# Kernel tuning notes

Hardware: AMD Instinct MI355X
Metric: run time of the kernel (lower is better)

Reference implementation:

```python
import jax, jax.numpy as jnp
import numpy as np

B, T, D_MODEL, N_HEAD = 2, 2048, 1024, 16
HEAD_DIM = D_MODEL // N_HEAD


def setup_inputs() -> dict:
    key = jax.random.key(0)
    ks = jax.random.split(key, 4)
    s = 0.02
    return {
        "x": jax.random.normal(ks[0], (B, T, D_MODEL), dtype=jnp.float32),
        "freqs_cis": jnp.zeros((T, HEAD_DIM // 2), dtype=jnp.float32),  # unused under ALiBi
        "Wq": jax.random.normal(ks[1], (D_MODEL, D_MODEL), dtype=jnp.float32) * s,
        "bq": jnp.zeros((D_MODEL,), dtype=jnp.float32),
        "Wkv": jax.random.normal(ks[2], (2 * D_MODEL, D_MODEL), dtype=jnp.float32) * s,
        "bkv": jnp.zeros((2 * D_MODEL,), dtype=jnp.float32),
        "Wo": jax.random.normal(ks[3], (D_MODEL, D_MODEL), dtype=jnp.float32) * s,
        "bo": jnp.zeros((D_MODEL,), dtype=jnp.float32),
    }


def reference(x, freqs_cis, Wq, bq, Wkv, bkv, Wo, bo):
    Bb, Tt, C = x.shape
    H, Dh = N_HEAD, HEAD_DIM
    # projections (torch Linear: x @ W^T + b)
    q = (x @ Wq.T + bq).reshape(Bb, Tt, H, Dh).transpose(0, 2, 1, 3)      # [B,H,T,Dh]
    kv = (x @ Wkv.T + bkv).reshape(Bb, Tt, 2, H, Dh).transpose(2, 0, 3, 1, 4)
    k, v = kv[0], kv[1]                                                    # [B,H,T,Dh]
    scores = jnp.einsum('bhqd,bhkd->bhqk', q, k) * (1.0 / np.sqrt(Dh))
    # ALiBi: linear slopes (1/H ... 1.0), bias = slope * (j - i)
    slopes = jnp.arange(1, H + 1, dtype=jnp.float32) / H                   # [H]
    pos = jnp.arange(Tt, dtype=jnp.float32)
    dist = pos[None, :] - pos[:, None]                                     # [T,T], j - i
    scores = scores + slopes[:, None, None] * dist[None]                   # broadcast over B
    # causal mask (upper triangle -> -inf)
    causal = pos[:, None] >= pos[None, :]                                  # [T,T] keep-mask
    scores = jnp.where(causal[None, None], scores, -jnp.inf)
    attn = jax.nn.softmax(scores, axis=-1)
    y = jnp.einsum('bhqk,bhkd->bhqd', attn, v)                             # [B,H,T,Dh]
    y = y.transpose(0, 2, 1, 3).reshape(Bb, Tt, C)
    return y @ Wo.T + bo
```

## Files before the change

kernel.cpp:

```cpp
#include <hip/hip_runtime.h>

typedef unsigned short u16;
typedef __bf16 bf16x8 __attribute__((ext_vector_type(8)));
typedef unsigned short u16x8 __attribute__((ext_vector_type(8)));
typedef float f32x4 __attribute__((ext_vector_type(4)));

#define KEY(r) ((((r) ^ ((r) >> 3)) & 7) << 3)
#define GP 72
#define VKEY(d) ((((d) >> 3) & 7) << 3)

static __device__ __forceinline__ u16 f2b(float f) {
  union { float f; unsigned u; } x; x.f = f;
  unsigned r = x.u + 0x7FFFu + ((x.u >> 16) & 1u);
  return (u16)(r >> 16);
}

static __device__ __forceinline__ float b2f(u16 s) {
  union { unsigned u; float f; } z; z.u = (unsigned)s << 16; return z.f;
}

static __device__ __forceinline__ bf16x8 ld_frag(const u16* p) {
  union { u16x8 s; bf16x8 b; } u;
  u.s = *reinterpret_cast<const u16x8*>(p);
  return u.b;
}

__global__ __launch_bounds__(256) void cvt_f32_bf16(const float* __restrict__ in,
                                                    u16* __restrict__ out, int n4) {
  int i = blockIdx.x * 256 + threadIdx.x;
  if (i >= n4) return;
  float4 v = reinterpret_cast<const float4*>(in)[i];
  ushort4 o;
  o.x = f2b(v.x); o.y = f2b(v.y); o.z = f2b(v.z); o.w = f2b(v.w);
  reinterpret_cast<ushort4*>(out)[i] = o;
}

template <bool OUT_BF16, int BN>
static __device__ __forceinline__ void gemm_body(
    const u16* __restrict__ A, const u16* __restrict__ Bt,
    const float* __restrict__ bias, void* __restrict__ outp,
    int N, int K, int row0, int col0, float scale) {
  constexpr int NF = BN / 32;
  __shared__ alignas(16) u16 As[128 * 64];
  __shared__ alignas(16) u16 Bs[BN * 64];
  const int tid = threadIdx.x, wid = tid >> 6, lane = tid & 63;
  const int wr = wid >> 1, wc = wid & 1;
  const int lr = lane >> 3;
  const int lc = (lane & 7) * 8;
  const int frow = lane & 15, fk = (lane >> 4) * 8;
  f32x4 acc[4][NF] = {};

  for (int k0 = 0; k0 < K; k0 += 64) {
    __syncthreads();
#pragma unroll
    for (int t = 0; t < 4; ++t) {
      const int r = wid * 32 + t * 8 + lr;
      __builtin_amdgcn_global_load_lds(
          (const __attribute__((address_space(1))) unsigned int*)(
              A + (size_t)(row0 + r) * K + k0 + (lc ^ KEY(r))),
          (__attribute__((address_space(3))) unsigned int*)(As + (wid * 32 + t * 8) * 64),
          16, 0, 0);
    }
#pragma unroll
    for (int t = 0; t < NF; ++t) {
      const int r = wid * (BN / 4) + t * 8 + lr;
      __builtin_amdgcn_global_load_lds(
          (const __attribute__((address_space(1))) unsigned int*)(
              Bt + (size_t)(col0 + r) * K + k0 + (lc ^ KEY(r))),
          (__attribute__((address_space(3))) unsigned int*)(Bs + (wid * (BN / 4) + t * 8) * 64),
          16, 0, 0);
    }
    __syncthreads();
#pragma unroll
    for (int ks = 0; ks < 2; ++ks) {
      bf16x8 a[4], b[NF];
#pragma unroll
      for (int m = 0; m < 4; ++m) {
        const int r = wr * 64 + m * 16 + frow;
        a[m] = ld_frag(&As[r * 64 + ((ks * 32 + fk) ^ KEY(r))]);
      }
#pragma unroll
      for (int n = 0; n < NF; ++n) {
        const int r = wc * (BN / 2) + n * 16 + frow;
        b[n] = ld_frag(&Bs[r * 64 + ((ks * 32 + fk) ^ KEY(r))]);
      }
#pragma unroll
      for (int m = 0; m < 4; ++m)
#pragma unroll
        for (int n = 0; n < NF; ++n)
          acc[m][n] = __builtin_amdgcn_mfma_f32_16x16x32_bf16(a[m], b[n], acc[m][n], 0, 0, 0);
    }
  }
  const int colL = lane & 15, rb = (lane >> 4) * 4;
#pragma unroll
  for (int n = 0; n < NF; ++n) {
    const int gc = col0 + wc * (BN / 2) + n * 16 + colL;
    const float bv = bias[gc];
#pragma unroll
    for (int m = 0; m < 4; ++m)
#pragma unroll
      for (int r = 0; r < 4; ++r) {
        const int gr = row0 + wr * 64 + m * 16 + rb + r;
        const float v = (acc[m][n][r] + bv) * scale;
        if constexpr (OUT_BF16)
          reinterpret_cast<u16*>(outp)[(size_t)gr * N + gc] = f2b(v);
        else
          reinterpret_cast<float*>(outp)[(size_t)gr * N + gc] = v;
      }
  }
}

__global__ __launch_bounds__(256) void gemm_qkv(
    const u16* __restrict__ xb, const u16* __restrict__ wqb,
    const u16* __restrict__ wkvb, const float* __restrict__ bq,
    const float* __restrict__ bkv, u16* __restrict__ qb, u16* __restrict__ kvb) {
  const int row0 = blockIdx.x * 128;
  const int by = blockIdx.y;
  const u16* Bt; const float* bias; u16* out; int N, col0; float scale;
  if (by < 8) { Bt = wqb;  bias = bq;  out = qb;  N = 1024; col0 = by * 128;      scale = 0.125f; }
  else        { Bt = wkvb; bias = bkv; out = kvb; N = 2048; col0 = (by - 8) * 128; scale = 1.0f; }
  gemm_body<true, 128>(xb, Bt, bias, out, N, 1024, row0, col0, scale);
}

__global__ __launch_bounds__(256) void gemm_o(
    const u16* __restrict__ yb, const u16* __restrict__ wob,
    const float* __restrict__ bo, float* __restrict__ out) {
  gemm_body<false, 64>(yb, wob, bo, out, 1024, 1024, blockIdx.x * 128, blockIdx.y * 64, 1.0f);
}

__global__ __launch_bounds__(256) void attn_split(
    const u16* __restrict__ qb,
    const u16* __restrict__ kvb,
    u16* __restrict__ yb,
    char* __restrict__ part,
    int T) {
  const int C = 1024;
  const int bh = blockIdx.x;
  const int b = bh >> 4, h = bh & 15;
  const float slope = (float)(h + 1) * 0.0625f;
  const int tid = threadIdx.x, wid = tid >> 6, lane = tid & 63;

  const int y = blockIdx.y;
  int qt, t0, t1, pidx; bool direct;
  if (y < 32) {
    qt = 31 - (y >> 1);
    const int c = y & 1, nt = qt + 1, half = (nt + 1) >> 1;
    t0 = c ? half : 0; t1 = c ? nt : half;
    direct = false;
    pidx = ((bh << 4) + (qt - 16)) * 2 + c;
  } else {
    qt = 47 - y; t0 = 0; t1 = qt + 1; direct = true; pidx = 0;
  }
  const int qBase = qt * 64;

  __shared__ alignas(16) u16 Ks[64 * GP];
  __shared__ alignas(16) u16 Vt[64 * GP];
  __shared__ alignas(16) u16 Ps[4][16 * GP];

  const int frow = lane & 15, fk = (lane >> 4) * 8;
  const int col = lane & 15, rb = (lane >> 4) * 4;

  const int q_row = qBase + wid * 16 + frow;
  const u16* qp = qb + (size_t)(b * T + q_row) * C + h * 64;
  const bf16x8 aq0 = ld_frag(qp + fk);
  const bf16x8 aq1 = ld_frag(qp + 32 + fk);

  float mrow[4] = {-1e30f, -1e30f, -1e30f, -1e30f};
  float lrow[4] = {0.f, 0.f, 0.f, 0.f};
  f32x4 accO[4] = {};

  const int sr = tid >> 3;
  const int sc = (tid & 7) * 8;

  for (int kt = t0; kt < t1; ++kt) {
    const int kBase = kt * 64;
    __syncthreads();
    {
      const size_t g0 = (size_t)(b * T + kBase + sr) * 2048 + h * 64 + sc;
      const size_t g1 = (size_t)(b * T + kBase + sr + 32) * 2048 + h * 64 + sc;
      *reinterpret_cast<int4*>(&Ks[sr * GP + sc]) = *reinterpret_cast<const int4*>(&kvb[g0]);
      *reinterpret_cast<int4*>(&Ks[(sr + 32) * GP + sc]) = *reinterpret_cast<const int4*>(&kvb[g1]);
      int4 v0 = *reinterpret_cast<const int4*>(&kvb[g0 + 1024]);
      int4 v1 = *reinterpret_cast<const int4*>(&kvb[g1 + 1024]);
      const u16* p0 = reinterpret_cast<const u16*>(&v0);
      const u16* p1 = reinterpret_cast<const u16*>(&v1);
      const int kx = VKEY(sc);
#pragma unroll
      for (int j = 0; j < 8; ++j) {
        const int d = sc + j;
        Vt[d * GP + (sr ^ kx)] = p0[j];
        Vt[d * GP + ((sr + 32) ^ kx)] = p1[j];
      }
    }
    __syncthreads();

    f32x4 accS[4] = {};
#pragma unroll
    for (int n = 0; n < 4; ++n) {
      bf16x8 bk0 = ld_frag(&Ks[(n * 16 + frow) * GP + fk]);
      accS[n] = __builtin_amdgcn_mfma_f32_16x16x32_bf16(aq0, bk0, accS[n], 0, 0, 0);
      bf16x8 bk1 = ld_frag(&Ks[(n * 16 + frow) * GP + 32 + fk]);
      accS[n] = __builtin_amdgcn_mfma_f32_16x16x32_bf16(aq1, bk1, accS[n], 0, 0, 0);
    }

#pragma unroll
    for (int r = 0; r < 4; ++r) {
      const int qg = qBase + wid * 16 + rb + r;
      float s[4];
      float tmax = -1e30f;
#pragma unroll
      for (int n = 0; n < 4; ++n) {
        const int kg = kBase + n * 16 + col;
        float v = accS[n][r] + slope * (float)(kg - qg);
        if (kg > qg) v = -1e30f;
        s[n] = v;
        tmax = fmaxf(tmax, v);
      }
      tmax = fmaxf(tmax, __shfl_xor(tmax, 1));
      tmax = fmaxf(tmax, __shfl_xor(tmax, 2));
      tmax = fmaxf(tmax, __shfl_xor(tmax, 4));
      tmax = fmaxf(tmax, __shfl_xor(tmax, 8));
      const float newm = fmaxf(mrow[r], tmax);
      const float corr = __expf(mrow[r] - newm);
      mrow[r] = newm;
      float psum = 0.f;
#pragma unroll
      for (int n = 0; n < 4; ++n) {
        const float p = __expf(s[n] - newm);
        psum += p;
        Ps[wid][(rb + r) * GP + n * 16 + col] = f2b(p);
      }
      psum += __shfl_xor(psum, 1);
      psum += __shfl_xor(psum, 2);
      psum += __shfl_xor(psum, 4);
      psum += __shfl_xor(psum, 8);
      lrow[r] = lrow[r] * corr + psum;
#pragma unroll
      for (int n = 0; n < 4; ++n) accO[n][r] *= corr;
    }

#pragma unroll
    for (int ks = 0; ks < 2; ++ks) {
      bf16x8 ap = ld_frag(&Ps[wid][frow * GP + ks * 32 + fk]);
#pragma unroll
      for (int n = 0; n < 4; ++n) {
        const int d = n * 16 + frow;
        bf16x8 bv = ld_frag(&Vt[d * GP + ((ks * 32 + fk) ^ VKEY(d))]);
        accO[n] = __builtin_amdgcn_mfma_f32_16x16x32_bf16(ap, bv, accO[n], 0, 0, 0);
      }
    }
  }

  if (direct) {
#pragma unroll
    for (int r = 0; r < 4; ++r) {
      const float inv = 1.0f / lrow[r];
      const int qg = qBase + wid * 16 + rb + r;
      u16* yrow = yb + (size_t)(b * T + qg) * C + h * 64;
#pragma unroll
      for (int n = 0; n < 4; ++n) yrow[n * 16 + col] = f2b(accO[n][r] * inv);
    }
  } else {
    u16* Orec = (u16*)(part + (size_t)pidx * 8704);
    float* mrec = (float*)(part + (size_t)pidx * 8704 + 8192);
#pragma unroll
    for (int r = 0; r < 4; ++r) {
      const int row = wid * 16 + rb + r;
#pragma unroll
      for (int n = 0; n < 4; ++n)
        Orec[row * 64 + n * 16 + col] = f2b(accO[n][r]);
      if (col == 0) { mrec[row] = mrow[r]; mrec[64 + row] = lrow[r]; }
    }
  }
}

__global__ __launch_bounds__(256) void attn_combine(
    const char* __restrict__ part, u16* __restrict__ yb, int T) {
  const int C = 1024;
  const int bh = blockIdx.x, b = bh >> 4, h = bh & 15;
  const int qt = 16 + blockIdx.y;
  const int tid = threadIdx.x;
  const int row = tid >> 2;
  const int d0 = (tid & 3) * 16;
  const size_t base = (size_t)(((bh << 4) + (qt - 16)) * 2) * 8704;
  const char* r0 = part + base;
  const char* r1 = part + base + 8704;
  const float m0 = ((const float*)(r0 + 8192))[row];
  const float l0 = ((const float*)(r0 + 8192))[64 + row];
  const float m1 = ((const float*)(r1 + 8192))[row];
  const float l1 = ((const float*)(r1 + 8192))[64 + row];
  const float M = fmaxf(m0, m1);
  const float w0 = __expf(m0 - M), w1 = __expf(m1 - M);
  const float inv = 1.0f / (l0 * w0 + l1 * w1);
  const u16* o0 = (const u16*)r0 + row * 64 + d0;
  const u16* o1 = (const u16*)r1 + row * 64 + d0;
  alignas(16) u16 outv[16];
#pragma unroll
  for (int j = 0; j < 16; ++j)
    outv[j] = f2b((b2f(o0[j]) * w0 + b2f(o1[j]) * w1) * inv);
  u16* yrow = yb + (size_t)(b * T + qt * 64 + row) * C + h * 64 + d0;
  *reinterpret_cast<int4*>(yrow) = *reinterpret_cast<const int4*>(outv);
  *reinterpret_cast<int4*>(yrow + 8) = *reinterpret_cast<const int4*>(outv + 8);
}

extern "C" void kernel_launch(void* const* d_in, const int* in_sizes, int n_in,
                              void* d_out, int out_size, void* d_ws, size_t ws_size,
                              hipStream_t stream) {
  const float* x   = (const float*)d_in[0];
  const float* Wq  = (const float*)d_in[2];
  const float* bq  = (const float*)d_in[3];
  const float* Wkv = (const float*)d_in[4];
  const float* bkv = (const float*)d_in[5];
  const float* Wo  = (const float*)d_in[6];
  const float* bo  = (const float*)d_in[7];
  float* out = (float*)d_out;

  const int B = 2, T = 2048, C = 1024;
  const int M = B * T;

  char* ws = (char*)d_ws;
  u16* xb   = (u16*)(ws + 0);
  u16* wqb  = (u16*)(ws + 8388608);
  u16* wkvb = (u16*)(ws + 10485760);
  u16* wob  = (u16*)(ws + 14680064);
  u16* qb   = (u16*)(ws + 16777216);
  u16* kvb  = (u16*)(ws + 25165824);
  u16* yb   = (u16*)(ws + 41943040);
  char* part = ws;

  cvt_f32_bf16<<<(M * C / 4 + 255) / 256, 256, 0, stream>>>(x, xb, M * C / 4);
  cvt_f32_bf16<<<(C * C / 4 + 255) / 256, 256, 0, stream>>>(Wq, wqb, C * C / 4);
  cvt_f32_bf16<<<(2 * C * C / 4 + 255) / 256, 256, 0, stream>>>(Wkv, wkvb, 2 * C * C / 4);
  cvt_f32_bf16<<<(C * C / 4 + 255) / 256, 256, 0, stream>>>(Wo, wob, C * C / 4);

  gemm_qkv<<<dim3(M / 128, 8 + 16), 256, 0, stream>>>(xb, wqb, wkvb, bq, bkv, qb, kvb);
  attn_split<<<dim3(B * 16, 48), 256, 0, stream>>>(qb, kvb, yb, part, T);
  attn_combine<<<dim3(B * 16, 16), 256, 0, stream>>>(part, yb, T);
  gemm_o<<<dim3(M / 128, C / 64), 256, 0, stream>>>(yb, wob, bo, out);
}
```

Measured before the change: 243.2 us.

## Transpose score MFMA to per-lane query rows and drop split-K combine

The score MFMA now takes swapped operands so each lane owns a single query row. Row max and sum then need only two cross-lane shuffles, and the bf16 P tile is packed into 32-bit shared-memory words instead of being stored one element at a time. The ALiBi term drops the -slope*q part, which is constant per row and cancels in softmax. The split-KV path plus its separate combine kernel are removed and replaced by one block per query tile, which brings back load imbalance on the long causal tiles in exchange for dropping the partial writes and an extra launch.

New measurement: 213.8 us. -12.1%, faster.

```diff
diff --git a/kernel.cpp b/kernel.cpp
--- a/kernel.cpp
+++ b/kernel.cpp
@@ -1,6 +1,7 @@
 #include <hip/hip_runtime.h>
 
 typedef unsigned short u16;
+typedef unsigned int u32;
 typedef __bf16 bf16x8 __attribute__((ext_vector_type(8)));
 typedef unsigned short u16x8 __attribute__((ext_vector_type(8)));
 typedef float f32x4 __attribute__((ext_vector_type(4)));
@@ -13,10 +14,6 @@
   union { float f; unsigned u; } x; x.f = f;
   unsigned r = x.u + 0x7FFFu + ((x.u >> 16) & 1u);
   return (u16)(r >> 16);
-}
-
-static __device__ __forceinline__ float b2f(u16 s) {
-  union { unsigned u; float f; } z; z.u = (unsigned)s << 16; return z.f;
 }
 
 static __device__ __forceinline__ bf16x8 ld_frag(const u16* p) {
@@ -128,51 +125,41 @@
   gemm_body<false, 64>(yb, wob, bo, out, 1024, 1024, blockIdx.x * 128, blockIdx.y * 64, 1.0f);
 }
 
-__global__ __launch_bounds__(256) void attn_split(
+__global__ __launch_bounds__(256) void attn_kernel(
     const u16* __restrict__ qb,
     const u16* __restrict__ kvb,
     u16* __restrict__ yb,
-    char* __restrict__ part,
     int T) {
   const int C = 1024;
   const int bh = blockIdx.x;
+  const int qt = (int)gridDim.y - 1 - (int)blockIdx.y;
   const int b = bh >> 4, h = bh & 15;
   const float slope = (float)(h + 1) * 0.0625f;
   const int tid = threadIdx.x, wid = tid >> 6, lane = tid & 63;
-
-  const int y = blockIdx.y;
-  int qt, t0, t1, pidx; bool direct;
-  if (y < 32) {
-    qt = 31 - (y >> 1);
-    const int c = y & 1, nt = qt + 1, half = (nt + 1) >> 1;
-    t0 = c ? half : 0; t1 = c ? nt : half;
-    direct = false;
-    pidx = ((bh << 4) + (qt - 16)) * 2 + c;
-  } else {
-    qt = 47 - y; t0 = 0; t1 = qt + 1; direct = true; pidx = 0;
-  }
   const int qBase = qt * 64;
 
   __shared__ alignas(16) u16 Ks[64 * GP];
   __shared__ alignas(16) u16 Vt[64 * GP];
-  __shared__ alignas(16) u16 Ps[4][16 * GP];
-
-  const int frow = lane & 15, fk = (lane >> 4) * 8;
-  const int col = lane & 15, rb = (lane >> 4) * 4;
-
-  const int q_row = qBase + wid * 16 + frow;
+  __shared__ alignas(16) u32 Pl[4][16 * 40];
+
+  const int qc = lane & 15;
+  const int g  = lane >> 4;
+  const int g4 = g * 4;
+  const int fk = g * 8;
+
+  const int q_row = qBase + wid * 16 + qc;
   const u16* qp = qb + (size_t)(b * T + q_row) * C + h * 64;
   const bf16x8 aq0 = ld_frag(qp + fk);
   const bf16x8 aq1 = ld_frag(qp + 32 + fk);
-
-  float mrow[4] = {-1e30f, -1e30f, -1e30f, -1e30f};
-  float lrow[4] = {0.f, 0.f, 0.f, 0.f};
+  const int qg = q_row;
+
+  float m_q = -1e30f, l_q = 0.f;
   f32x4 accO[4] = {};
 
   const int sr = tid >> 3;
   const int sc = (tid & 7) * 8;
 
-  for (int kt = t0; kt < t1; ++kt) {
+  for (int kt = 0; kt <= qt; ++kt) {
     const int kBase = kt * 64;
     __syncthreads();
     {
@@ -197,110 +184,84 @@
     f32x4 accS[4] = {};
 #pragma unroll
     for (int n = 0; n < 4; ++n) {
-      bf16x8 bk0 = ld_frag(&Ks[(n * 16 + frow) * GP + fk]);
-      accS[n] = __builtin_amdgcn_mfma_f32_16x16x32_bf16(aq0, bk0, accS[n], 0, 0, 0);
-      bf16x8 bk1 = ld_frag(&Ks[(n * 16 + frow) * GP + 32 + fk]);
-      accS[n] = __builtin_amdgcn_mfma_f32_16x16x32_bf16(aq1, bk1, accS[n], 0, 0, 0);
-    }
-
-#pragma unroll
-    for (int r = 0; r < 4; ++r) {
-      const int qg = qBase + wid * 16 + rb + r;
-      float s[4];
-      float tmax = -1e30f;
+      bf16x8 bk0 = ld_frag(&Ks[(n * 16 + qc) * GP + fk]);
+      accS[n] = __builtin_amdgcn_mfma_f32_16x16x32_bf16(bk0, aq0, accS[n], 0, 0, 0);
+      bf16x8 bk1 = ld_frag(&Ks[(n * 16 + qc) * GP + 32 + fk]);
+      accS[n] = __builtin_amdgcn_mfma_f32_16x16x32_bf16(bk1, aq1, accS[n], 0, 0, 0);
+    }
+
+    float tmax = -1e30f;
+#pragma unroll
+    for (int n = 0; n < 4; ++n) {
+      const int kgn = kBase + n * 16 + g4;
+#pragma unroll
+      for (int r = 0; r < 4; ++r) {
+        const int kg = kgn + r;
+        float v = fmaf(slope, (float)kg, accS[n][r]);
+        v = (kg > qg) ? -1e30f : v;
+        accS[n][r] = v;
+        tmax = fmaxf(tmax, v);
+      }
+    }
+    tmax = fmaxf(tmax, __shfl_xor(tmax, 16));
+    tmax = fmaxf(tmax, __shfl_xor(tmax, 32));
+    const float newm = fmaxf(m_q, tmax);
+    const float corr = __expf(m_q - newm);
+    m_q = newm;
+    float psum = 0.f;
+#pragma unroll
+    for (int n = 0; n < 4; ++n)
+#pragma unroll
+      for (int r = 0; r < 4; ++r) {
+        const float p = __expf(accS[n][r] - newm);
+        accS[n][r] = p;
+        psum += p;
+      }
+    psum += __shfl_xor(psum, 16);
+    psum += __shfl_xor(psum, 32);
+    l_q = l_q * corr + psum;
+
+    u32* Pw = &Pl[wid][qc * 40];
+#pragma unroll
+    for (int n = 0; n < 4; ++n) {
+      union { float f; u32 u; } a0, a1, a2, a3;
+      a0.f = accS[n][0]; a1.f = accS[n][1]; a2.f = accS[n][2]; a3.f = accS[n][3];
+      u32 w0 = (a0.u >> 16) | (a1.u & 0xFFFF0000u);
+      u32 w1 = (a2.u >> 16) | (a3.u & 0xFFFF0000u);
+      *reinterpret_cast<uint2*>(&Pw[8 * n + 2 * g]) = uint2{w0, w1};
+    }
+
+    float corr4[4];
+#pragma unroll
+    for (int r = 0; r < 4; ++r) corr4[r] = __shfl(corr, g4 + r);
+#pragma unroll
+    for (int n = 0; n < 4; ++n)
+#pragma unroll
+      for (int r = 0; r < 4; ++r) accO[n][r] *= corr4[r];
+
+#pragma unroll
+    for (int ks = 0; ks < 2; ++ks) {
+      uint4 pv4 = *reinterpret_cast<const uint4*>(&Pl[wid][qc * 40 + 16 * ks + g4]);
+      union { uint4 q; u16x8 s; bf16x8 bv; } ap; ap.q = pv4;
 #pragma unroll
       for (int n = 0; n < 4; ++n) {
-        const int kg = kBase + n * 16 + col;
-        float v = accS[n][r] + slope * (float)(kg - qg);
-        if (kg > qg) v = -1e30f;
-        s[n] = v;
-        tmax = fmaxf(tmax, v);
-      }
-      tmax = fmaxf(tmax, __shfl_xor(tmax, 1));
-      tmax = fmaxf(tmax, __shfl_xor(tmax, 2));
-      tmax = fmaxf(tmax, __shfl_xor(tmax, 4));
-      tmax = fmaxf(tmax, __shfl_xor(tmax, 8));
-      const float newm = fmaxf(mrow[r], tmax);
-      const float corr = __expf(mrow[r] - newm);
-      mrow[r] = newm;
-      float psum = 0.f;
-#pragma unroll
-      for (int n = 0; n < 4; ++n) {
-        const float p = __expf(s[n] - newm);
-        psum += p;
-        Ps[wid][(rb + r) * GP + n * 16 + col] = f2b(p);
-      }
-      psum += __shfl_xor(psum, 1);
-      psum += __shfl_xor(psum, 2);
-      psum += __shfl_xor(psum, 4);
-      psum += __shfl_xor(psum, 8);
-      lrow[r] = lrow[r] * corr + psum;
-#pragma unroll
-      for (int n = 0; n < 4; ++n) accO[n][r] *= corr;
-    }
-
-#pragma unroll
-    for (int ks = 0; ks < 2; ++ks) {
-      bf16x8 ap = ld_frag(&Ps[wid][frow * GP + ks * 32 + fk]);
-#pragma unroll
-      for (int n = 0; n < 4; ++n) {
-        const int d = n * 16 + frow;
+        const int d = n * 16 + qc;
         bf16x8 bv = ld_frag(&Vt[d * GP + ((ks * 32 + fk) ^ VKEY(d))]);
-        accO[n] = __builtin_amdgcn_mfma_f32_16x16x32_bf16(ap, bv, accO[n], 0, 0, 0);
-      }
-    }
-  }
-
-  if (direct) {
-#pragma unroll
-    for (int r = 0; r < 4; ++r) {
-      const float inv = 1.0f / lrow[r];
-      const int qg = qBase + wid * 16 + rb + r;
-      u16* yrow = yb + (size_t)(b * T + qg) * C + h * 64;
-#pragma unroll
-      for (int n = 0; n < 4; ++n) yrow[n * 16 + col] = f2b(accO[n][r] * inv);
-    }
-  } else {
-    u16* Orec = (u16*)(part + (size_t)pidx * 8704);
-    float* mrec = (float*)(part + (size_t)pidx * 8704 + 8192);
-#pragma unroll
-    for (int r = 0; r < 4; ++r) {
-      const int row = wid * 16 + rb + r;
-#pragma unroll
-      for (int n = 0; n < 4; ++n)
-        Orec[row * 64 + n * 16 + col] = f2b(accO[n][r]);
-      if (col == 0) { mrec[row] = mrow[r]; mrec[64 + row] = lrow[r]; }
-    }
-  }
-}
-
-__global__ __launch_bounds__(256) void attn_combine(
-    const char* __restrict__ part, u16* __restrict__ yb, int T) {
-  const int C = 1024;
-  const int bh = blockIdx.x, b = bh >> 4, h = bh & 15;
-  const int qt = 16 + blockIdx.y;
-  const int tid = threadIdx.x;
-  const int row = tid >> 2;
-  const int d0 = (tid & 3) * 16;
-  const size_t base = (size_t)(((bh << 4) + (qt - 16)) * 2) * 8704;
-  const char* r0 = part + base;
-  const char* r1 = part + base + 8704;
-  const float m0 = ((const float*)(r0 + 8192))[row];
-  const float l0 = ((const float*)(r0 + 8192))[64 + row];
-  const float m1 = ((const float*)(r1 + 8192))[row];
-  const float l1 = ((const float*)(r1 + 8192))[64 + row];
-  const float M = fmaxf(m0, m1);
-  const float w0 = __expf(m0 - M), w1 = __expf(m1 - M);
-  const float inv = 1.0f / (l0 * w0 + l1 * w1);
-  const u16* o0 = (const u16*)r0 + row * 64 + d0;
-  const u16* o1 = (const u16*)r1 + row * 64 + d0;
-  alignas(16) u16 outv[16];
-#pragma unroll
-  for (int j = 0; j < 16; ++j)
-    outv[j] = f2b((b2f(o0[j]) * w0 + b2f(o1[j]) * w1) * inv);
-  u16* yrow = yb + (size_t)(b * T + qt * 64 + row) * C + h * 64 + d0;
-  *reinterpret_cast<int4*>(yrow) = *reinterpret_cast<const int4*>(outv);
-  *reinterpret_cast<int4*>(yrow + 8) = *reinterpret_cast<const int4*>(outv + 8);
+        accO[n] = __builtin_amdgcn_mfma_f32_16x16x32_bf16(ap.bv, bv, accO[n], 0, 0, 0);
+      }
+    }
+  }
+
+  float inv4[4];
+#pragma unroll
+  for (int r = 0; r < 4; ++r) inv4[r] = 1.0f / __shfl(l_q, g4 + r);
+#pragma unroll
+  for (int r = 0; r < 4; ++r) {
+    const int qg2 = qBase + wid * 16 + g4 + r;
+    u16* yrow = yb + (size_t)(b * T + qg2) * C + h * 64;
+#pragma unroll
+    for (int n = 0; n < 4; ++n) yrow[n * 16 + qc] = f2b(accO[n][r] * inv4[r]);
+  }
 }
 
 extern "C" void kernel_launch(void* const* d_in, const int* in_sizes, int n_in,
@@ -326,7 +287,6 @@
   u16* qb   = (u16*)(ws + 16777216);
   u16* kvb  = (u16*)(ws + 25165824);
   u16* yb   = (u16*)(ws + 41943040);
-  char* part = ws;
 
   cvt_f32_bf16<<<(M * C / 4 + 255) / 256, 256, 0, stream>>>(x, xb, M * C / 4);
   cvt_f32_bf16<<<(C * C / 4 + 255) / 256, 256, 0, stream>>>(Wq, wqb, C * C / 4);
@@ -334,7 +294,6 @@
   cvt_f32_bf16<<<(C * C / 4 + 255) / 256, 256, 0, stream>>>(Wo, wob, C * C / 4);
 
   gemm_qkv<<<dim3(M / 128, 8 + 16), 256, 0, stream>>>(xb, wqb, wkvb, bq, bkv, qb, kvb);
-  attn_split<<<dim3(B * 16, 48), 256, 0, stream>>>(qb, kvb, yb, part, T);
-  attn_combine<<<dim3(B * 16, 16), 256, 0, stream>>>(part, yb, T);
+  attn_kernel<<<dim3(B * 16, T / 64), 256, 0, stream>>>(qb, kvb, yb, T);
   gemm_o<<<dim3(M / 128, C / 64), 256, 0, stream>>>(yb, wob, bo, out);
 }
```
